# Performance work log

Measured on AMD Instinct MI355X. Metric: run time of the kernel, lower is better.

## Reference

```python
import jax, jax.numpy as jnp
import numpy as np

C_IN = 256
C_INTER = 128
B, H, W = 8, 64, 64
EPS = 1e-5


def setup_inputs() -> dict:
    key = jax.random.key(0)
    ks = jax.random.split(key, 12)
    s = 0.02
    return {
        "x": jax.random.normal(ks[0], (B, C_IN, H, W), dtype=jnp.float32),
        "bn_gamma": jnp.ones((C_IN,), jnp.float32),
        "bn_beta": jnp.zeros((C_IN,), jnp.float32),
        "bn_mean": jax.random.normal(ks[1], (C_IN,), jnp.float32) * 0.1,
        "bn_var": jnp.abs(jax.random.normal(ks[2], (C_IN,), jnp.float32)) * 0.1 + 1.0,
        "w_g": jax.random.normal(ks[3], (C_INTER, C_IN), jnp.float32) * s,
        "b_g": jnp.zeros((C_INTER,), jnp.float32),
        "w_theta": jax.random.normal(ks[4], (C_INTER, C_IN), jnp.float32) * s,
        "b_theta": jnp.zeros((C_INTER,), jnp.float32),
        "w_phi": jax.random.normal(ks[5], (C_INTER, C_IN), jnp.float32) * s,
        "b_phi": jnp.zeros((C_INTER,), jnp.float32),
        "w_w": jax.random.normal(ks[6], (C_IN, C_INTER), jnp.float32) * s,
        "b_w": jnp.zeros((C_IN,), jnp.float32),
    }


def reference(x, bn_gamma, bn_beta, bn_mean, bn_var,
              w_g, b_g, w_theta, b_theta, w_phi, b_phi, w_w, b_w):
    b, c, h, w = x.shape
    # BatchNorm2d (inference form, running stats) -- self.bn in the original
    scale = bn_gamma * jax.lax.rsqrt(bn_var + EPS)
    xb = x * scale[None, :, None, None] + (bn_beta - bn_mean * scale)[None, :, None, None]
    xf = xb.reshape(b, c, h * w)  # (B, C, N); conv1x1 == channel matmul
    g = jnp.einsum('oc,bcn->bon', w_g, xf) + b_g[None, :, None]          # (B, Ci, N)
    th = jnp.einsum('oc,bcn->bon', w_theta, xf) + b_theta[None, :, None]  # (B, Ci, N)
    ph = jnp.einsum('oc,bcn->bon', w_phi, xf) + b_phi[None, :, None]      # (B, Ci, N)
    f = jnp.einsum('bcn,bcm->bnm', th, ph)  # (B, N, N), NO 1/sqrt(d) scaling
    a = jax.nn.softmax(f, axis=-1)
    y = jnp.einsum('bnm,bcm->bcn', a, g)    # (B, Ci, N)
    wy = jnp.einsum('oc,bcn->bon', w_w, y) + b_w[None, :, None]  # (B, C, N)
    return wy.reshape(b, c, h, w) + x
```

## Files before the change

kernel.cpp:

```cpp
#include <hip/hip_runtime.h>
#include <hip/hip_bf16.h>
#include <stdint.h>

#define BB   8
#define CIN  256
#define CI   128
#define NN   4096
#define EPSV 1e-5f
#define LOG2E 1.44269504088896340736f

typedef __attribute__((ext_vector_type(8))) short bf16x8;
typedef __attribute__((ext_vector_type(4))) short bf16x4;
typedef __attribute__((ext_vector_type(4))) float f32x4;
typedef __attribute__((ext_vector_type(2))) float f32x2;
typedef __attribute__((ext_vector_type(2))) unsigned int u32x2;

static __device__ inline short f2bf(float f) {
    uint32_t u = __builtin_bit_cast(uint32_t, f);
    u += 0x7FFFu + ((u >> 16) & 1u);
    return (short)(u >> 16);
}

static __device__ inline float bf2f(short s) {
    uint32_t u = ((uint32_t)(uint16_t)s) << 16;
    return __builtin_bit_cast(float, u);
}

static __device__ inline uint32_t cvt_pk_bf16(float lo, float hi) {
    uint32_t r;
    asm("v_cvt_pk_bf16_f32 %0, %1, %2" : "=v"(r) : "v"(lo), "v"(hi));
    return r;
}

__global__ __launch_bounds__(256) void prep_kernel(
    const float* __restrict__ wth, const float* __restrict__ wph,
    const float* __restrict__ wg,  const float* __restrict__ ww,
    short* __restrict__ wq, short* __restrict__ wwb)
{
    int t = blockIdx.x * 256 + threadIdx.x;
    if (t < 12288) {
        int s  = t >> 12;
        int r  = t & 4095;
        int o  = r >> 5;
        int j  = r & 31;
        int k  = j >> 3, jj = j & 7;
        const float* W = (s == 0) ? wth : (s == 1) ? wph : wg;
        float sc = (s == 0) ? LOG2E : 1.0f;
        const float* src = &W[(size_t)o * CIN + k * 64 + jj * 8];
        bf16x8 d;
        #pragma unroll
        for (int i = 0; i < 8; ++i) d[i] = f2bf(src[i] * sc);
        size_t doff = (size_t)s * 65536 + (size_t)k * 16384
                    + (size_t)o * 128 + (size_t)((jj ^ (o & 7)) << 4);
        *(bf16x8*)((char*)wq + doff) = d;
    } else if (t < 16384) {
        int r = t - 12288;
        int o = r >> 4, j = r & 15;
        const float* src = &ww[(size_t)o * CI + j * 8];
        bf16x8 d;
        #pragma unroll
        for (int i = 0; i < 8; ++i) d[i] = f2bf(src[i]);
        *(bf16x8*)&wwb[(size_t)o * CI + j * 8] = d;
    }
}

__global__ __launch_bounds__(256, 2) void proj_kernel(
    const float* __restrict__ x,
    const float* __restrict__ gamma, const float* __restrict__ beta,
    const float* __restrict__ mean,  const float* __restrict__ var,
    const short* __restrict__ wq,
    const float* __restrict__ bth, const float* __restrict__ bph,
    const float* __restrict__ bg,
    short* __restrict__ qp, short* __restrict__ kp, short* __restrict__ vtp)
{
    __shared__ float s_scale[CIN];
    __shared__ float s_shift[CIN];
    __shared__ __align__(16) short A_lds[64][264];
    __shared__ __align__(16) char  B_sh[2][128 * 128];

    const int tid = threadIdx.x;
    const int b   = blockIdx.x & 7;
    const int n0  = (blockIdx.x >> 3) * 64;
    const int w = tid >> 6, lane = tid & 63, lr = lane & 15, lg = lane >> 4;

    {
        float sc = gamma[tid] * rsqrtf(var[tid] + EPSV);
        s_scale[tid] = sc;
        s_shift[tid] = beta[tid] - mean[tid] * sc;
    }
    __syncthreads();

    #pragma unroll
    for (int p = 0; p < 8; ++p) {
        int c2 = p * 32 + (tid >> 4) * 2;
        int n4 = (tid & 15) * 4;
        f32x4 v0 = *(const f32x4*)&x[((size_t)b * CIN + c2) * NN + n0 + n4];
        f32x4 v1 = *(const f32x4*)&x[((size_t)b * CIN + c2 + 1) * NN + n0 + n4];
        float sc0 = s_scale[c2],     sh0 = s_shift[c2];
        float sc1 = s_scale[c2 + 1], sh1 = s_shift[c2 + 1];
        #pragma unroll
        for (int i = 0; i < 4; ++i) {
            uint32_t pk = cvt_pk_bf16(v0[i] * sc0 + sh0, v1[i] * sc1 + sh1);
            *(uint32_t*)&A_lds[n4 + i][c2] = pk;
        }
    }

    auto stageB = [&](int buf, int idx) {
        const char* src = (const char*)wq + (size_t)idx * 16384;
        #pragma unroll
        for (int r = 0; r < 4; ++r) {
            __builtin_amdgcn_global_load_lds(
                (const __attribute__((address_space(1))) void*)
                    (src + ((((r * 4 + w) << 6) + lane) << 4)),
                (__attribute__((address_space(3))) void*)&B_sh[buf][(r * 4 + w) << 10],
                16, 0, 0);
        }
    };
    stageB(0, 0);
    __syncthreads();

    const float* BS[3] = {bth, bph, bg};
    f32x4 acc[8];

    for (int idx = 0; idx < 12; ++idx) {
        const int s = idx >> 2, k = idx & 3, buf = idx & 1;
        if (idx + 1 < 12) stageB(buf ^ 1, idx + 1);

        if (k == 0) {
            #pragma unroll
            for (int i = 0; i < 8; ++i) acc[i] = (f32x4){0.f, 0.f, 0.f, 0.f};
        }
        const int c0 = k * 64;
        bf16x8 a0 = *(const bf16x8*)&A_lds[w * 16 + lr][c0 + lg * 8];
        bf16x8 a1 = *(const bf16x8*)&A_lds[w * 16 + lr][c0 + 32 + lg * 8];
        const char* Bc = B_sh[buf];
        #pragma unroll
        for (int ot = 0; ot < 8; ++ot) {
            const int o  = ot * 16 + lr;
            const int sw = (o & 7) << 4;
            bf16x8 b0 = *(const bf16x8*)(Bc + o * 128 + ((lg << 4) ^ sw));
            bf16x8 b1 = *(const bf16x8*)(Bc + o * 128 + (((4 + lg) << 4) ^ sw));
            acc[ot] = __builtin_amdgcn_mfma_f32_16x16x32_bf16(a0, b0, acc[ot], 0, 0, 0);
            acc[ot] = __builtin_amdgcn_mfma_f32_16x16x32_bf16(a1, b1, acc[ot], 0, 0, 0);
        }

        if (k == 3) {
            if (s < 2) {
                short* dst = (s == 0) ? qp : kp;
                const float om = (s == 0) ? LOG2E : 1.0f;
                #pragma unroll
                for (int ot = 0; ot < 8; ++ot) {
                    float bias = BS[s][ot * 16 + lr] * om;
                    #pragma unroll
                    for (int rr = 0; rr < 4; ++rr) {
                        int n = n0 + w * 16 + lg * 4 + rr;
                        dst[((size_t)b * NN + n) * CI + ot * 16 + lr] = f2bf(acc[ot][rr] + bias);
                    }
                }
            } else {
                #pragma unroll
                for (int ot = 0; ot < 8; ++ot) {
                    float bias = BS[s][ot * 16 + lr];
                    bf16x4 pk;
                    #pragma unroll
                    for (int rr = 0; rr < 4; ++rr) pk[rr] = f2bf(acc[ot][rr] + bias);
                    *(bf16x4*)&vtp[((size_t)b * CI + ot * 16 + lr) * NN + n0 + w * 16 + lg * 4] = pk;
                }
            }
        }
        __syncthreads();
    }
}

__global__ __launch_bounds__(256, 2) void attn_kernel(
    const short* __restrict__ qp, const short* __restrict__ kp,
    const short* __restrict__ vtp, short* __restrict__ yh,
    float* __restrict__ ml)
{
    __shared__ __align__(16) char K_sh[2][64 * 256];
    __shared__ __align__(16) char V_sh[2][128 * 128];
    __shared__ __align__(16) char P_sh[4][16 * 128];

    const int tid  = threadIdx.x;
    const int b    = blockIdx.x & 7;
    const int half = (blockIdx.x >> 3) & 1;
    const int n0   = (blockIdx.x >> 4) * 128;
    const int w = tid >> 6, lane = tid & 63, lr = lane & 15, lg = lane >> 4;
    const int NT = NN / 128;
    const int t0 = half * NT;

    const char* kgp[4];
    const char* vgp[4];
    #pragma unroll
    for (int r = 0; r < 4; ++r) {
        int idx = ((r * 4 + w) << 6) + lane;
        int mm  = idx >> 4, cb = (idx & 15) << 4;
        kgp[r] = (const char*)(kp + (size_t)b * NN * CI + (size_t)t0 * 64 * CI
                               + (size_t)mm * CI) + (cb ^ ((mm & 7) << 4));
        int cc = idx >> 3, cbv = (idx & 7) << 4;
        vgp[r] = (const char*)(vtp + (size_t)b * CI * NN + (size_t)t0 * 64
                               + (size_t)cc * NN) + (cbv ^ ((cc & 7) << 4));
    }
    auto stage = [&](int bufi) {
        #pragma unroll
        for (int r = 0; r < 4; ++r) {
            __builtin_amdgcn_global_load_lds(
                (const __attribute__((address_space(1))) void*)kgp[r],
                (__attribute__((address_space(3))) void*)&K_sh[bufi][(r * 4 + w) << 10],
                16, 0, 0);
            __builtin_amdgcn_global_load_lds(
                (const __attribute__((address_space(1))) void*)vgp[r],
                (__attribute__((address_space(3))) void*)&V_sh[bufi][(r * 4 + w) << 10],
                16, 0, 0);
            kgp[r] += 64 * CI * 2;
            vgp[r] += 64 * 2;
        }
    };

    bf16x8 qf[2][4];
    #pragma unroll
    for (int s = 0; s < 2; ++s) {
        const short* qrow = qp + ((size_t)b * NN + n0 + w * 32 + s * 16 + lr) * CI;
        #pragma unroll
        for (int kf = 0; kf < 4; ++kf)
            qf[s][kf] = *(const bf16x8*)&qrow[kf * 32 + lg * 8];
    }

    f32x4 yacc[2][8];
    #pragma unroll
    for (int s = 0; s < 2; ++s)
        #pragma unroll
        for (int i = 0; i < 8; ++i) yacc[s][i] = (f32x4){0.f, 0.f, 0.f, 0.f};
    float m_run[2] = {-__builtin_huge_valf(), -__builtin_huge_valf()};
    float l_run[2] = {0.f, 0.f};

    stage(0);
    __syncthreads();

    for (int t = 0; t < NT; ++t) {
        const int cur = t & 1;
        if (t + 1 < NT) stage(cur ^ 1);

        const char* Kc = K_sh[cur];
        f32x4 sa[2][4];
        __builtin_amdgcn_s_setprio(1);
        #pragma unroll
        for (int mt = 0; mt < 4; ++mt) {
            const int mrow = mt * 16 + lr;
            const int sw   = (mrow & 7) << 4;
            sa[0][mt] = (f32x4){0.f, 0.f, 0.f, 0.f};
            sa[1][mt] = (f32x4){0.f, 0.f, 0.f, 0.f};
            #pragma unroll
            for (int kf = 0; kf < 4; ++kf) {
                bf16x8 kfrag = *(const bf16x8*)(Kc + (mrow << 8) + ((kf * 64 + lg * 16) ^ sw));
                sa[0][mt] = __builtin_amdgcn_mfma_f32_16x16x32_bf16(kfrag, qf[0][kf], sa[0][mt], 0, 0, 0);
                sa[1][mt] = __builtin_amdgcn_mfma_f32_16x16x32_bf16(kfrag, qf[1][kf], sa[1][mt], 0, 0, 0);
            }
        }
        __builtin_amdgcn_s_setprio(0);

        float tml[2];
        #pragma unroll
        for (int s = 0; s < 2; ++s) {
            float tm = fmaxf(fmaxf(fmaxf(sa[s][0][0], sa[s][0][1]), fmaxf(sa[s][0][2], sa[s][0][3])),
                             fmaxf(fmaxf(sa[s][1][0], sa[s][1][1]), fmaxf(sa[s][1][2], sa[s][1][3])));
            tm = fmaxf(tm, fmaxf(fmaxf(fmaxf(sa[s][2][0], sa[s][2][1]), fmaxf(sa[s][2][2], sa[s][2][3])),
                                 fmaxf(fmaxf(sa[s][3][0], sa[s][3][1]), fmaxf(sa[s][3][2], sa[s][3][3]))));
            tml[s] = tm;
        }
        if (__any((tml[0] - m_run[0] > 8.f) || (tml[1] - m_run[1] > 8.f))) {
            #pragma unroll
            for (int s = 0; s < 2; ++s) {
                float tm = tml[s];
                tm = fmaxf(tm, __shfl_xor(tm, 16));
                tm = fmaxf(tm, __shfl_xor(tm, 32));
                float mnew = fmaxf(m_run[s], tm);
                float sc   = __builtin_amdgcn_exp2f(m_run[s] - mnew);
                m_run[s] = mnew;
                l_run[s] *= sc;
                #pragma unroll
                for (int rr = 0; rr < 4; ++rr) {
                    float scb = __shfl(sc, (lane & 48) | (lg * 4 + rr));
                    #pragma unroll
                    for (int ct = 0; ct < 8; ++ct) yacc[s][ct][rr] *= scb;
                }
            }
        }

        const char* Vc = V_sh[cur];
        bf16x8 vf[2][8];
        #pragma unroll
        for (int kf = 0; kf < 2; ++kf)
            #pragma unroll
            for (int ct = 0; ct < 8; ++ct) {
                const int vr = ct * 16 + lr;
                vf[kf][ct] = *(const bf16x8*)(Vc + (vr << 7) +
                                              ((kf * 64 + lg * 16) ^ ((vr & 7) << 4)));
            }

        char* Pb = P_sh[w];
        const int psw = (lr & 7) << 4;
        bf16x8 pa0[2], pa1[2];
        {
            float rs = 0.f;
            #pragma unroll
            for (int mt = 0; mt < 4; ++mt) {
                float e0 = __builtin_amdgcn_exp2f(sa[0][mt][0] - m_run[0]);
                float e1 = __builtin_amdgcn_exp2f(sa[0][mt][1] - m_run[0]);
                float e2 = __builtin_amdgcn_exp2f(sa[0][mt][2] - m_run[0]);
                float e3 = __builtin_amdgcn_exp2f(sa[0][mt][3] - m_run[0]);
                rs += (e0 + e1) + (e2 + e3);
                u32x2 pk = {cvt_pk_bf16(e0, e1), cvt_pk_bf16(e2, e3)};
                *(u32x2*)(Pb + lr * 128 + ((mt * 32 + lg * 8) ^ psw)) = pk;
            }
            l_run[0] += rs;
        }
        asm volatile("" ::: "memory");
        #pragma unroll
        for (int kf = 0; kf < 2; ++kf)
            pa0[kf] = *(const bf16x8*)(Pb + lr * 128 + ((kf * 64 + lg * 16) ^ psw));
        asm volatile("" ::: "memory");

        {
            float rs = 0.f;
            #pragma unroll
            for (int mt = 0; mt < 4; ++mt) {
                float e0 = __builtin_amdgcn_exp2f(sa[1][mt][0] - m_run[1]);
                float e1 = __builtin_amdgcn_exp2f(sa[1][mt][1] - m_run[1]);
                float e2 = __builtin_amdgcn_exp2f(sa[1][mt][2] - m_run[1]);
                float e3 = __builtin_amdgcn_exp2f(sa[1][mt][3] - m_run[1]);
                rs += (e0 + e1) + (e2 + e3);
                u32x2 pk = {cvt_pk_bf16(e0, e1), cvt_pk_bf16(e2, e3)};
                *(u32x2*)(Pb + lr * 128 + ((mt * 32 + lg * 8) ^ psw)) = pk;
            }
            l_run[1] += rs;
        }
        asm volatile("" ::: "memory");
        #pragma unroll
        for (int kf = 0; kf < 2; ++kf)
            pa1[kf] = *(const bf16x8*)(Pb + lr * 128 + ((kf * 64 + lg * 16) ^ psw));

        __builtin_amdgcn_s_setprio(1);
        #pragma unroll
        for (int kf = 0; kf < 2; ++kf)
            #pragma unroll
            for (int ct = 0; ct < 8; ++ct) {
                yacc[0][ct] = __builtin_amdgcn_mfma_f32_16x16x32_bf16(pa0[kf], vf[kf][ct], yacc[0][ct], 0, 0, 0);
                yacc[1][ct] = __builtin_amdgcn_mfma_f32_16x16x32_bf16(pa1[kf], vf[kf][ct], yacc[1][ct], 0, 0, 0);
            }
        __builtin_amdgcn_s_setprio(0);

        __syncthreads();
    }

    #pragma unroll
    for (int s = 0; s < 2; ++s) {
        float lt = l_run[s];
        lt += __shfl_xor(lt, 16);
        lt += __shfl_xor(lt, 32);
        l_run[s] = lt;
    }

    short* yb = yh + ((size_t)half * BB + b) * NN * (size_t)CI;
    #pragma unroll
    for (int s = 0; s < 2; ++s) {
        #pragma unroll
        for (int rr = 0; rr < 4; ++rr) {
            int n = n0 + w * 32 + s * 16 + lg * 4 + rr;
            #pragma unroll
            for (int ct = 0; ct < 8; ++ct)
                yb[(size_t)n * CI + ct * 16 + lr] = f2bf(yacc[s][ct][rr]);
        }
    }
    if (lg == 0) {
        #pragma unroll
        for (int s = 0; s < 2; ++s) {
            int n = n0 + w * 32 + s * 16 + lr;
            f32x2 v = {m_run[s], l_run[s]};
            *(f32x2*)&ml[(((size_t)half * BB + b) * NN + n) * 2] = v;
        }
    }
}

__global__ __launch_bounds__(256) void merge_kernel(
    const short* __restrict__ yh, const float* __restrict__ ml,
    short* __restrict__ yp)
{
    const int tid = threadIdx.x;
    const int row = blockIdx.x * 8 + (tid >> 5);
    const int c4  = (tid & 31) * 4;
    const size_t H = (size_t)BB * NN * CI;
    const size_t R = (size_t)BB * NN * 2;

    float m0 = ml[(size_t)row * 2],     l0 = ml[(size_t)row * 2 + 1];
    float m1 = ml[R + (size_t)row * 2], l1 = ml[R + (size_t)row * 2 + 1];
    float mm = fmaxf(m0, m1);
    float w0 = __builtin_amdgcn_exp2f(m0 - mm);
    float w1 = __builtin_amdgcn_exp2f(m1 - mm);
    float inv = 1.0f / (l0 * w0 + l1 * w1);
    w0 *= inv; w1 *= inv;

    bf16x4 a  = *(const bf16x4*)&yh[(size_t)row * CI + c4];
    bf16x4 bb = *(const bf16x4*)&yh[H + (size_t)row * CI + c4];
    bf16x4 o;
    #pragma unroll
    for (int i = 0; i < 4; ++i) o[i] = f2bf(bf2f(a[i]) * w0 + bf2f(bb[i]) * w1);
    *(bf16x4*)&yp[(size_t)row * CI + c4] = o;
}

template <int MERGED>
__global__ __launch_bounds__(256) void out_kernel(
    const short* __restrict__ ysrc, const float* __restrict__ ml,
    const short* __restrict__ wwb, const float* __restrict__ bw,
    const float* __restrict__ x, float* __restrict__ out)
{
    __shared__ __align__(16) short A_lds[128][136];
    __shared__ __align__(16) short Bl[128][136];

    const int tid  = threadIdx.x;
    const int b    = blockIdx.x & 7;
    const int rest = blockIdx.x >> 3;
    const int ob   = rest & 1;
    const int nn   = (rest >> 1) * 128;
    const int o0   = ob * 128;
    const int w = tid >> 6, lane = tid & 63, lr = lane & 15, lg = lane >> 4;

    #pragma unroll
    for (int pass = 0; pass < 8; ++pass) {
        int o  = pass * 16 + (tid >> 4);
        int c8 = (tid & 15) * 8;
        *(bf16x8*)&A_lds[o][c8] = *(const bf16x8*)&wwb[(size_t)(o0 + o) * CI + c8];
    }
    #pragma unroll
    for (int pass = 0; pass < 8; ++pass) {
        int n  = pass * 16 + (tid >> 4);
        int c8 = (tid & 15) * 8;
        size_t row = (size_t)b * NN + nn + n;
        if (MERGED) {
            *(bf16x8*)&Bl[n][c8] = *(const bf16x8*)&ysrc[row * CI + c8];
        } else {
            const size_t H = (size_t)BB * NN * CI;
            const size_t R = (size_t)BB * NN * 2;
            f32x2 v0 = *(const f32x2*)&ml[row * 2];
            f32x2 v1 = *(const f32x2*)&ml[R + row * 2];
            float mm = fmaxf(v0[0], v1[0]);
            float w0 = __builtin_amdgcn_exp2f(v0[0] - mm);
            float w1 = __builtin_amdgcn_exp2f(v1[0] - mm);
            float inv = 1.0f / (v0[1] * w0 + v1[1] * w1);
            w0 *= inv; w1 *= inv;
            bf16x8 a  = *(const bf16x8*)&ysrc[row * CI + c8];
            bf16x8 b2 = *(const bf16x8*)&ysrc[H + row * CI + c8];
            bf16x8 ov;
            #pragma unroll
            for (int i = 0; i < 4; ++i) {
                float lo = bf2f(a[2*i]) * w0 + bf2f(b2[2*i]) * w1;
                float hi = bf2f(a[2*i+1]) * w0 + bf2f(b2[2*i+1]) * w1;
                uint32_t pk = cvt_pk_bf16(lo, hi);
                ov[2*i]   = (short)(pk & 0xFFFF);
                ov[2*i+1] = (short)(pk >> 16);
            }
            *(bf16x8*)&Bl[n][c8] = ov;
        }
    }
    __syncthreads();

    f32x4 acc[2][8];
    #pragma unroll
    for (int i = 0; i < 2; ++i)
        #pragma unroll
        for (int j = 0; j < 8; ++j) acc[i][j] = (f32x4){0.f, 0.f, 0.f, 0.f};

    #pragma unroll
    for (int kf = 0; kf < 4; ++kf) {
        bf16x8 a0 = *(const bf16x8*)&A_lds[w * 32 + lr][kf * 32 + lg * 8];
        bf16x8 a1 = *(const bf16x8*)&A_lds[w * 32 + 16 + lr][kf * 32 + lg * 8];
        #pragma unroll
        for (int nt = 0; nt < 8; ++nt) {
            bf16x8 bv = *(const bf16x8*)&Bl[nt * 16 + lr][kf * 32 + lg * 8];
            acc[0][nt] = __builtin_amdgcn_mfma_f32_16x16x32_bf16(a0, bv, acc[0][nt], 0, 0, 0);
            acc[1][nt] = __builtin_amdgcn_mfma_f32_16x16x32_bf16(a1, bv, acc[1][nt], 0, 0, 0);
        }
    }

    #pragma unroll
    for (int wo = 0; wo < 2; ++wo) {
        #pragma unroll
        for (int rr = 0; rr < 4; ++rr) {
            int o = o0 + w * 32 + wo * 16 + lg * 4 + rr;
            float bias = bw[o];
            #pragma unroll
            for (int nt = 0; nt < 8; ++nt) {
                size_t idx = ((size_t)b * CIN + o) * NN + nn + nt * 16 + lr;
                out[idx] = acc[wo][nt][rr] + bias + x[idx];
            }
        }
    }
}

extern "C" void kernel_launch(void* const* d_in, const int* in_sizes, int n_in,
                              void* d_out, int out_size, void* d_ws, size_t ws_size,
                              hipStream_t stream)
{
    const float* x     = (const float*)d_in[0];
    const float* gamma = (const float*)d_in[1];
    const float* beta  = (const float*)d_in[2];
    const float* mean  = (const float*)d_in[3];
    const float* var   = (const float*)d_in[4];
    const float* wg    = (const float*)d_in[5];
    const float* bg    = (const float*)d_in[6];
    const float* wth   = (const float*)d_in[7];
    const float* bth   = (const float*)d_in[8];
    const float* wph   = (const float*)d_in[9];
    const float* bph   = (const float*)d_in[10];
    const float* ww    = (const float*)d_in[11];
    const float* bw    = (const float*)d_in[12];

    const size_t seg = (size_t)BB * NN * CI;
    short* qp  = (short*)d_ws;
    short* kp  = qp + seg;
    short* vtp = kp + seg;
    float* ml  = (float*)(vtp + seg);
    short* wq  = (short*)((char*)d_ws + 25690112);
    short* wwb = (short*)((char*)d_ws + 25690112 + 196608);
    const size_t yh_off = 25u * 1024 * 1024;
    const bool fused = ws_size >= yh_off + 2 * seg * sizeof(short);
    short* yh = fused ? (short*)((char*)d_ws + yh_off) : (short*)d_out;
    (void)in_sizes; (void)n_in; (void)out_size;

    prep_kernel<<<64, 256, 0, stream>>>(wth, wph, wg, ww, wq, wwb);
    proj_kernel<<<BB * (NN / 64), 256, 0, stream>>>(
        x, gamma, beta, mean, var, wq, bth, bph, bg, qp, kp, vtp);
    attn_kernel<<<2 * BB * (NN / 128), 256, 0, stream>>>(qp, kp, vtp, yh, ml);
    if (fused) {
        out_kernel<0><<<2 * BB * (NN / 128), 256, 0, stream>>>(
            yh, ml, wwb, bw, x, (float*)d_out);
    } else {
        short* yp = qp;
        merge_kernel<<<BB * NN / 8, 256, 0, stream>>>(yh, ml, yp);
        out_kernel<1><<<2 * BB * (NN / 128), 256, 0, stream>>>(
            yp, ml, wwb, bw, x, (float*)d_out);
    }
}
```

Baseline: 116.4 us.

## Store Q and K in FP8 and compute QK^T with scaled FP8 MFMA

The projection kernel now writes the theta and phi projections as FP8 (e4m3) bytes instead of bf16. The attention kernel stages half as many K bytes into LDS and computes the scores with a single 16x16x128 f8f6f4 scaled MFMA per tile, replacing four bf16 MFMAs. This cuts K/Q memory traffic, LDS footprint and MFMA count in the score stage. In exchange the scores lose precision, and because there is no 1/sqrt(d) scaling that error feeds directly into the softmax, so accuracy may suffer.

```diff
diff --git a/kernel.cpp b/kernel.cpp
--- a/kernel.cpp
+++ b/kernel.cpp
@@ -14,6 +14,8 @@
 typedef __attribute__((ext_vector_type(4))) float f32x4;
 typedef __attribute__((ext_vector_type(2))) float f32x2;
 typedef __attribute__((ext_vector_type(2))) unsigned int u32x2;
+typedef __attribute__((ext_vector_type(4))) int i32x4;
+typedef __attribute__((ext_vector_type(8))) int i32x8;
 
 static __device__ inline short f2bf(float f) {
     uint32_t u = __builtin_bit_cast(uint32_t, f);
@@ -71,7 +73,8 @@
     const short* __restrict__ wq,
     const float* __restrict__ bth, const float* __restrict__ bph,
     const float* __restrict__ bg,
-    short* __restrict__ qp, short* __restrict__ kp, short* __restrict__ vtp)
+    unsigned char* __restrict__ qp, unsigned char* __restrict__ kp,
+    short* __restrict__ vtp)
 {
     __shared__ float s_scale[CIN];
     __shared__ float s_shift[CIN];
@@ -146,7 +149,7 @@
 
         if (k == 3) {
             if (s < 2) {
-                short* dst = (s == 0) ? qp : kp;
+                unsigned char* dst = (s == 0) ? qp : kp;
                 const float om = (s == 0) ? LOG2E : 1.0f;
                 #pragma unroll
                 for (int ot = 0; ot < 8; ++ot) {
@@ -154,7 +157,10 @@
                     #pragma unroll
                     for (int rr = 0; rr < 4; ++rr) {
                         int n = n0 + w * 16 + lg * 4 + rr;
-                        dst[((size_t)b * NN + n) * CI + ot * 16 + lr] = f2bf(acc[ot][rr] + bias);
+                        uint32_t pk = __builtin_amdgcn_cvt_pk_fp8_f32(
+                            acc[ot][rr] + bias, 0.f, 0, false);
+                        dst[((size_t)b * NN + n) * 128 + ot * 16 + lr] =
+                            (unsigned char)(pk & 0xFF);
                     }
                 }
             } else {
@@ -173,11 +179,11 @@
 }
 
 __global__ __launch_bounds__(256, 2) void attn_kernel(
-    const short* __restrict__ qp, const short* __restrict__ kp,
+    const unsigned char* __restrict__ qp, const unsigned char* __restrict__ kp,
     const short* __restrict__ vtp, short* __restrict__ yh,
     float* __restrict__ ml)
 {
-    __shared__ __align__(16) char K_sh[2][64 * 256];
+    __shared__ __align__(16) char K_sh[2][64 * 128];
     __shared__ __align__(16) char V_sh[2][128 * 128];
     __shared__ __align__(16) char P_sh[4][16 * 128];
 
@@ -189,41 +195,48 @@
     const int NT = NN / 128;
     const int t0 = half * NT;
 
-    const char* kgp[4];
+    const unsigned char* kgp[2];
     const char* vgp[4];
+    #pragma unroll
+    for (int r = 0; r < 2; ++r) {
+        int idx = ((r * 4 + w) << 6) + lane;
+        int mm  = idx >> 3, cb = (idx & 7) << 4;
+        kgp[r] = kp + (size_t)b * NN * 128 + (size_t)(t0 * 64 + mm) * 128
+               + (cb ^ ((mm & 7) << 4));
+    }
     #pragma unroll
     for (int r = 0; r < 4; ++r) {
         int idx = ((r * 4 + w) << 6) + lane;
-        int mm  = idx >> 4, cb = (idx & 15) << 4;
-        kgp[r] = (const char*)(kp + (size_t)b * NN * CI + (size_t)t0 * 64 * CI
-                               + (size_t)mm * CI) + (cb ^ ((mm & 7) << 4));
         int cc = idx >> 3, cbv = (idx & 7) << 4;
         vgp[r] = (const char*)(vtp + (size_t)b * CI * NN + (size_t)t0 * 64
                                + (size_t)cc * NN) + (cbv ^ ((cc & 7) << 4));
     }
     auto stage = [&](int bufi) {
         #pragma unroll
-        for (int r = 0; r < 4; ++r) {
+        for (int r = 0; r < 2; ++r) {
             __builtin_amdgcn_global_load_lds(
                 (const __attribute__((address_space(1))) void*)kgp[r],
                 (__attribute__((address_space(3))) void*)&K_sh[bufi][(r * 4 + w) << 10],
                 16, 0, 0);
+            kgp[r] += 64 * 128;
+        }
+        #pragma unroll
+        for (int r = 0; r < 4; ++r) {
             __builtin_amdgcn_global_load_lds(
                 (const __attribute__((address_space(1))) void*)vgp[r],
                 (__attribute__((address_space(3))) void*)&V_sh[bufi][(r * 4 + w) << 10],
                 16, 0, 0);
-            kgp[r] += 64 * CI * 2;
             vgp[r] += 64 * 2;
         }
     };
 
-    bf16x8 qf[2][4];
+    i32x8 qf8[2];
     #pragma unroll
     for (int s = 0; s < 2; ++s) {
-        const short* qrow = qp + ((size_t)b * NN + n0 + w * 32 + s * 16 + lr) * CI;
-        #pragma unroll
-        for (int kf = 0; kf < 4; ++kf)
-            qf[s][kf] = *(const bf16x8*)&qrow[kf * 32 + lg * 8];
+        const unsigned char* qrow = qp + ((size_t)b * NN + n0 + w * 32 + s * 16 + lr) * 128;
+        i32x4 lo = *(const i32x4*)(qrow + lg * 32);
+        i32x4 hi = *(const i32x4*)(qrow + lg * 32 + 16);
+        qf8[s] = (i32x8){lo[0], lo[1], lo[2], lo[3], hi[0], hi[1], hi[2], hi[3]};
     }
 
     f32x4 yacc[2][8];
@@ -248,14 +261,16 @@
         for (int mt = 0; mt < 4; ++mt) {
             const int mrow = mt * 16 + lr;
             const int sw   = (mrow & 7) << 4;
-            sa[0][mt] = (f32x4){0.f, 0.f, 0.f, 0.f};
-            sa[1][mt] = (f32x4){0.f, 0.f, 0.f, 0.f};
-            #pragma unroll
-            for (int kf = 0; kf < 4; ++kf) {
-                bf16x8 kfrag = *(const bf16x8*)(Kc + (mrow << 8) + ((kf * 64 + lg * 16) ^ sw));
-                sa[0][mt] = __builtin_amdgcn_mfma_f32_16x16x32_bf16(kfrag, qf[0][kf], sa[0][mt], 0, 0, 0);
-                sa[1][mt] = __builtin_amdgcn_mfma_f32_16x16x32_bf16(kfrag, qf[1][kf], sa[1][mt], 0, 0, 0);
-            }
+            const char* kr = Kc + mrow * 128;
+            i32x4 k0 = *(const i32x4*)(kr + ((lg * 32) ^ sw));
+            i32x4 k1 = *(const i32x4*)(kr + ((lg * 32 + 16) ^ sw));
+            i32x8 kf8 = (i32x8){k0[0], k0[1], k0[2], k0[3], k1[0], k1[1], k1[2], k1[3]};
+            sa[0][mt] = __builtin_amdgcn_mfma_scale_f32_16x16x128_f8f6f4(
+                kf8, qf8[0], (f32x4){0.f, 0.f, 0.f, 0.f},
+                0, 0, 0, 0x7F7F7F7F, 0, 0x7F7F7F7F);
+            sa[1][mt] = __builtin_amdgcn_mfma_scale_f32_16x16x128_f8f6f4(
+                kf8, qf8[1], (f32x4){0.f, 0.f, 0.f, 0.f},
+                0, 0, 0, 0x7F7F7F7F, 0, 0x7F7F7F7F);
         }
         __builtin_amdgcn_s_setprio(0);
 
@@ -516,10 +531,10 @@
     const float* bw    = (const float*)d_in[12];
 
     const size_t seg = (size_t)BB * NN * CI;
-    short* qp  = (short*)d_ws;
-    short* kp  = qp + seg;
-    short* vtp = kp + seg;
-    float* ml  = (float*)(vtp + seg);
+    unsigned char* qp = (unsigned char*)d_ws;
+    unsigned char* kp = (unsigned char*)d_ws + seg * sizeof(short);
+    short* vtp = (short*)((char*)d_ws + 2 * seg * sizeof(short));
+    float* ml  = (float*)((char*)d_ws + 3 * seg * sizeof(short));
     short* wq  = (short*)((char*)d_ws + 25690112);
     short* wwb = (short*)((char*)d_ws + 25690112 + 196608);
     const size_t yh_off = 25u * 1024 * 1024;
@@ -535,7 +550,7 @@
         out_kernel<0><<<2 * BB * (NN / 128), 256, 0, stream>>>(
             yh, ml, wwb, bw, x, (float*)d_out);
     } else {
-        short* yp = qp;
+        short* yp = (short*)d_ws;
         merge_kernel<<<BB * NN / 8, 256, 0, stream>>>(yh, ml, yp);
         out_kernel<1><<<2 * BB * (NN / 128), 256, 0, stream>>>(
             yp, ml, wwb, bw, x, (float*)d_out);
```

After: 103.5 us. 11.1% less time.
